# Kernel tuning notes

Measured on AMD Instinct MI355X. Metric: run time of the kernel, lower is better.

The kernel has to match this reference:

```python
import jax, jax.numpy as jnp
import numpy as np

D_MODEL = 2048
D_INNER = 4096
D_CONV = 4
D_STATE = 16
DT_RANK = 128  # (d_model + 15) // 16
EPS = 1e-5
B_SZ, SEQ = 2, 2048


def _silu(x):
    return x * jax.nn.sigmoid(x)


def setup_inputs() -> dict:
    key = jax.random.key(0)
    ks = jax.random.split(key, 10)
    s = lambda k, shape, sc=0.02: jax.random.normal(k, shape, jnp.float32) * sc
    # S4D-real init for A_log, small negative bias for dt (standard Mamba init)
    A_log = jnp.log(jnp.tile(jnp.arange(1, D_STATE + 1, dtype=jnp.float32), (D_INNER, 1)))
    return {
        "hidden_states": jax.random.normal(ks[0], (B_SZ, SEQ, D_MODEL), jnp.float32),
        "norm_scale": jnp.ones((D_MODEL,), jnp.float32),
        "in_proj_w": s(ks[1], (2 * D_INNER, D_MODEL)),
        "conv_w": s(ks[2], (D_INNER, 1, D_CONV), 0.1),
        "conv_b": s(ks[3], (D_INNER,), 0.1),
        "x_proj_w": s(ks[4], (DT_RANK + 2 * D_STATE, D_INNER)),
        "dt_proj_w": s(ks[5], (D_INNER, DT_RANK), 0.1),
        "dt_proj_b": jnp.full((D_INNER,), -4.0, jnp.float32) + s(ks[6], (D_INNER,), 0.1),
        "out_proj_w": s(ks[7], (D_MODEL, D_INNER)),
        "A_log": A_log,
        "D": jnp.ones((D_INNER,), jnp.float32),
    }


def reference(hidden_states, norm_scale, in_proj_w, conv_w, conv_b, x_proj_w,
              dt_proj_w, dt_proj_b, out_proj_w, A_log, D):
    B, L, _ = hidden_states.shape
    residual = hidden_states
    # RMSNorm
    rms = jnp.sqrt(jnp.mean(hidden_states ** 2, axis=-1, keepdims=True) + EPS)
    xn = hidden_states / rms * norm_scale
    # in_proj -> [B, L, 2*d_inner]; torch code keeps this as projected_states
    xz = jnp.einsum('bld,ed->ble', xn, in_proj_w)
    x_in = xz[..., :D_INNER].transpose(0, 2, 1)  # [B, d_inner, L]
    z = xz[..., D_INNER:]                        # [B, L, d_inner]
    # depthwise causal conv1d (padding d_conv-1, truncated to L) + SiLU
    xc = jax.lax.conv_general_dilated(
        x_in, conv_w, window_strides=(1,), padding=[(D_CONV - 1, 0)],
        feature_group_count=D_INNER)
    xc = _silu(xc + conv_b[None, :, None])       # [B, d_inner, L]
    # x_proj -> dt, B, C
    x_dbl = jnp.einsum('bdl,rd->brl', xc, x_proj_w)  # [B, dt_rank+2*d_state, L]
    dt_low = x_dbl[:, :DT_RANK]
    Bm = x_dbl[:, DT_RANK:DT_RANK + D_STATE]         # [B, d_state, L]
    Cm = x_dbl[:, DT_RANK + D_STATE:]                # [B, d_state, L]
    delta = jax.nn.softplus(
        jnp.einsum('dr,brl->bdl', dt_proj_w, dt_low) + dt_proj_b[None, :, None])
    A = -jnp.exp(A_log)                              # [d_inner, d_state]
    # selective scan: h_t = exp(delta_t * A) * h_{t-1} + delta_t * B_t * u_t
    delta_t = delta.transpose(2, 0, 1)  # [L, B, d_inner]
    u_t = xc.transpose(2, 0, 1)         # [L, B, d_inner]
    B_t = Bm.transpose(2, 0, 1)         # [L, B, d_state]
    C_t = Cm.transpose(2, 0, 1)         # [L, B, d_state]

    def step(h, inp):
        d_, b_, c_, u_ = inp
        dA = jnp.exp(d_[..., None] * A)                      # [B, d_inner, d_state]
        h = h * dA + (d_ * u_)[..., None] * b_[:, None, :]   # [B, d_inner, d_state]
        y = jnp.einsum('bds,bs->bd', h, c_)                  # [B, d_inner]
        return h, y

    h0 = jnp.zeros((B, D_INNER, D_STATE), hidden_states.dtype)
    _, ys = jax.lax.scan(step, h0, (delta_t, B_t, C_t, u_t))  # [L, B, d_inner]
    y = ys.transpose(1, 0, 2) + xc.transpose(0, 2, 1) * D     # [B, L, d_inner]
    y = y * _silu(z)
    out = jnp.einsum('bld,od->blo', y, out_proj_w)            # [B, L, d_model]
    return residual + out, xz
```

## Files before the change

### kernel.cpp

```cpp
#include <hip/hip_runtime.h>
#include <cstdint>
#include <cstddef>

#define DM   2048
#define DI   4096
#define DST  16
#define DTR  128
#define SEQL 2048
#define NTOK 4096
#define XZW  8192
#define NCHAIN 8192
#define CL   32
#define NCH  64

typedef short short8 __attribute__((ext_vector_type(8)));
typedef float f32x4 __attribute__((ext_vector_type(4)));

__device__ __forceinline__ short f2bf(float x) {
  union { float f; uint32_t u; } v; v.f = x;
  uint32_t r = v.u + 0x7fffu + ((v.u >> 16) & 1u);
  return (short)(r >> 16);
}
__device__ __forceinline__ float bf2f(short s) {
  union { uint32_t u; float f; } v; v.u = ((uint32_t)(uint16_t)s) << 16;
  return v.f;
}

__device__ __forceinline__ void stage16(const short* g, short* l) {
#if __has_builtin(__builtin_amdgcn_global_load_lds)
  __builtin_amdgcn_global_load_lds((const __attribute__((address_space(1))) void*)g,
                                   (__attribute__((address_space(3))) void*)l, 16, 0, 0);
#else
  *(short8*)l = *(const short8*)g;
#endif
}

#define NG_WIN  (XZW * DM / 4)
#define NG_WOUT (DM * DI / 4)
#define NG_WDT  (DI * DTR / 4)
#define NG_PAD  (256 * DI / 4)
#define NG_ALL  (NG_WIN + NG_WOUT + NG_WDT + NG_PAD)
#define NB_CVT  (NG_ALL / 256)
__global__ __launch_bounds__(256) void prep_k(const float* __restrict__ win,
                                              const float* __restrict__ wout,
                                              const float* __restrict__ wdt,
                                              const float* __restrict__ xp,
                                              const float* __restrict__ hs,
                                              const float* __restrict__ nsc,
                                              short* __restrict__ win_bf,
                                              short* __restrict__ wout_bf,
                                              short* __restrict__ wdt_bf,
                                              short* __restrict__ wxp_bf,
                                              short* __restrict__ xn_bf) {
  const int blk = blockIdx.x;
  const int tid = threadIdx.x;
  if (blk < NB_CVT) {
    const size_t i = (size_t)blk * 256 + tid;
    float4 v;
    short4* dst;
    if (i < NG_WIN) {
      v = ((const float4*)win)[i];
      dst = (short4*)win_bf + i;
    } else if (i < NG_WIN + NG_WOUT) {
      const size_t j = i - NG_WIN;
      v = ((const float4*)wout)[j];
      dst = (short4*)wout_bf + j;
    } else if (i < NG_WIN + NG_WOUT + NG_WDT) {
      const size_t j = i - NG_WIN - NG_WOUT;
      v = ((const float4*)wdt)[j];
      dst = (short4*)wdt_bf + j;
    } else {
      const size_t j = i - NG_WIN - NG_WOUT - NG_WDT;
      const int r = (int)(j >> 10);
      v = (r < 160) ? ((const float4*)xp)[j] : make_float4(0.f, 0.f, 0.f, 0.f);
      dst = (short4*)wxp_bf + j;
    }
    short4 o;
    o.x = f2bf(v.x); o.y = f2bf(v.y); o.z = f2bf(v.z); o.w = f2bf(v.w);
    *dst = o;
  } else {
    const int token = blk - NB_CVT;
    const float* row = hs + (size_t)token * DM;
    float4 a = ((const float4*)row)[tid];
    float4 b = ((const float4*)row)[tid + 256];
    float ss = a.x*a.x + a.y*a.y + a.z*a.z + a.w*a.w
             + b.x*b.x + b.y*b.y + b.z*b.z + b.w*b.w;
    #pragma unroll
    for (int o = 32; o > 0; o >>= 1) ss += __shfl_xor(ss, o);
    __shared__ float wsum[4];
    if ((tid & 63) == 0) wsum[tid >> 6] = ss;
    __syncthreads();
    float tot = wsum[0] + wsum[1] + wsum[2] + wsum[3];
    float inv = rsqrtf(tot * (1.0f / DM) + 1e-5f);
    float4 s1 = ((const float4*)nsc)[tid];
    float4 s2 = ((const float4*)nsc)[tid + 256];
    short4 o1, o2;
    o1.x = f2bf(a.x * inv * s1.x); o1.y = f2bf(a.y * inv * s1.y);
    o1.z = f2bf(a.z * inv * s1.z); o1.w = f2bf(a.w * inv * s1.w);
    o2.x = f2bf(b.x * inv * s2.x); o2.y = f2bf(b.y * inv * s2.y);
    o2.z = f2bf(b.z * inv * s2.z); o2.w = f2bf(b.w * inv * s2.w);
    ((short4*)xn_bf)[(size_t)token * (DM / 4) + tid] = o1;
    ((short4*)xn_bf)[(size_t)token * (DM / 4) + tid + 256] = o2;
  }
}

#define LGKM_FENCE() do { asm volatile("s_waitcnt lgkmcnt(0)" ::: "memory"); \
                          __builtin_amdgcn_sched_barrier(0); } while (0)

template <int RBY, int RBX>
__global__ __launch_bounds__(512) void gemm_big(const short* __restrict__ A,
                                                const short* __restrict__ B,
                                                int K, int ksz, int N, int nbx,
                                                float* __restrict__ out_f,
                                                size_t zstride) {
  constexpr int MFR = 8;
  constexpr int BM = 256;
  constexpr int ABYTES = BM * 128;
  constexpr int BBYTES = 256 * 128;
  constexpr int BUF = ABYTES + BBYTES;
  constexpr int FPP = 4;
  __shared__ char lds[2 * BUF];

  const int tid = threadIdx.x;
  const int lane = tid & 63;
  const int wid = tid >> 6;
  const int wm = wid >> 2;
  const int wn = wid & 3;
  const int lr = lane & 15;
  const int lj = lane >> 4;

  const int xcd = blockIdx.x & 7;
  const int idx = blockIdx.x >> 3;
  const int nrgx = nbx / RBX;
  const int by = (xcd / nrgx) * RBY + idx / RBX;
  const int bx = (xcd % nrgx) * RBX + idx % RBX;
  const size_t m0 = (size_t)by * BM;
  const size_t n0 = (size_t)bx * 256;

  const int kbase = blockIdx.y * ksz;
  out_f += (size_t)blockIdx.y * zstride;
  const int NT = ksz >> 6;

  auto stA1 = [&](int t, char* buf, int s) {
    const int k0 = kbase + (t << 6);
    const int off = s * 8192 + tid * 16;
    const int r = off >> 7;
    const int j = (off >> 4) & 7;
    stage16(A + (m0 + r) * (size_t)K + k0 + ((j ^ (r & 7)) << 3),
            (short*)(buf + off));
  };
  auto stB1 = [&](int t, char* buf, int s) {
    const int k0 = kbase + (t << 6);
    const int off = s * 8192 + tid * 16;
    const int r = off >> 7;
    const int j = (off >> 4) & 7;
    stage16(B + (n0 + r) * (size_t)K + k0 + ((j ^ (r & 7)) << 3),
            (short*)(buf + ABYTES + off));
  };

#define READ_A(dst, fbase)                                                   \
  _Pragma("unroll")                                                          \
  for (int f = 0; f < 4; ++f) {                                              \
    const int arow = wm * (BM / 2) + ((fbase) + f) * 16 + lr;                \
    _Pragma("unroll")                                                        \
    for (int ks = 0; ks < 2; ++ks)                                           \
      dst[f][ks] = *(const short8*)(cur + arow * 128 +                       \
                     ((((ks << 2) + lj) ^ (arow & 7)) << 4));                \
  }
#define READ_B(dst, gbase)                                                   \
  _Pragma("unroll")                                                          \
  for (int g = 0; g < 2; ++g) {                                              \
    const int brow = wn * 64 + ((gbase) + g) * 16 + lr;                      \
    _Pragma("unroll")                                                        \
    for (int ks = 0; ks < 2; ++ks)                                           \
      dst[g][ks] = *(const short8*)(cur + ABYTES + brow * 128 +              \
                     ((((ks << 2) + lj) ^ (brow & 7)) << 4));                \
  }
#define MFMA_Q(accoff, avoff, gbase, bvx)                                    \
  __builtin_amdgcn_s_setprio(1);                                             \
  _Pragma("unroll")                                                          \
  for (int ks = 0; ks < 2; ++ks)                                             \
    _Pragma("unroll")                                                        \
    for (int f = 0; f < FPP; ++f)                                            \
      _Pragma("unroll")                                                      \
      for (int g = 0; g < 2; ++g)                                            \
        acc[(accoff) + f][(gbase) + g] = __builtin_amdgcn_mfma_f32_16x16x32_bf16( \
            av[(avoff) + f][ks], bvx[g][ks], acc[(accoff) + f][(gbase) + g], 0, 0, 0); \
  __builtin_amdgcn_s_setprio(0);

  f32x4 acc[MFR][4] = {};

  {
    #pragma unroll
    for (int s = 0; s < 4; ++s) stA1(0, lds, s);
    #pragma unroll
    for (int s = 0; s < 4; ++s) stB1(0, lds, s);
    if (NT > 1) {
      stA1(1, lds + BUF, 0); stA1(1, lds + BUF, 2);
      asm volatile("s_waitcnt vmcnt(2)" ::: "memory");
    } else asm volatile("s_waitcnt vmcnt(0)" ::: "memory");
    __builtin_amdgcn_s_barrier();
    __builtin_amdgcn_sched_barrier(0);
  }

  for (int t = 0; t < NT; ++t) {
    char* cur = lds + (t & 1) * BUF;
    char* nxt = lds + ((t + 1) & 1) * BUF;
    const bool m1 = (t + 1) < NT;
    const bool m2 = (t + 2) < NT;
    short8 av[4][2], bv0[2][2], bv1[2][2];

    READ_A(av, 0);
    READ_B(bv0, 0);
    if (m1) { stA1(t + 1, nxt, 1); stA1(t + 1, nxt, 3); }
    LGKM_FENCE();
    MFMA_Q(0, 0, 0, bv0);
    __builtin_amdgcn_s_barrier();

    READ_B(bv1, 2);
    if (m1) { stB1(t + 1, nxt, 0); stB1(t + 1, nxt, 1); }
    LGKM_FENCE();
    MFMA_Q(0, 0, 2, bv1);
    __builtin_amdgcn_s_barrier();

    READ_A(av, 4);
    if (m1) { stB1(t + 1, nxt, 2); stB1(t + 1, nxt, 3); }
    if (m2) { stA1(t + 2, cur, 0); stA1(t + 2, cur, 2); }
    LGKM_FENCE();
    MFMA_Q(4, 0, 2, bv1);
    __builtin_amdgcn_s_barrier();

    MFMA_Q(4, 0, 0, bv0);
    if (m2) asm volatile("s_waitcnt vmcnt(2)" ::: "memory");
    else    asm volatile("s_waitcnt vmcnt(0)" ::: "memory");
    __builtin_amdgcn_s_barrier();
    __builtin_amdgcn_sched_barrier(0);
  }

  #pragma unroll
  for (int f = 0; f < MFR; ++f)
    #pragma unroll
    for (int g = 0; g < 4; ++g)
      #pragma unroll
      for (int jj = 0; jj < 4; ++jj) {
        const size_t row = m0 + wm * (BM / 2) + f * 16 + lj * 4 + jj;
        const size_t col = n0 + wn * 64 + g * 16 + lr;
        out_f[row * (size_t)N + col] = acc[f][g][jj];
      }
#undef READ_A
#undef READ_B
#undef MFMA_Q
}

__global__ __launch_bounds__(256) void combine_k(const float* __restrict__ part,
                                                 const float* __restrict__ hs,
                                                 float* __restrict__ out0) {
  const size_t i = (size_t)blockIdx.x * 256 + threadIdx.x;
  const float4 p0 = ((const float4*)part)[i];
  const float4 p1 = ((const float4*)part)[i + (size_t)NTOK * DM / 4];
  const float4 r  = ((const float4*)hs)[i];
  float4 o;
  o.x = r.x + p0.x + p1.x; o.y = r.y + p0.y + p1.y;
  o.z = r.z + p0.z + p1.z; o.w = r.w + p0.w + p1.w;
  ((float4*)out0)[i] = o;
}

template <int EPI>
__global__ __launch_bounds__(256) void gemm_nt(const short* __restrict__ A,
                                               const short* __restrict__ B,
                                               int ld, int K, int N,
                                               float* __restrict__ out_f,
                                               const float* __restrict__ aux_f,
                                               short* __restrict__ out_bf) {
  __shared__ short As[128 * 64];
  __shared__ short Bs[128 * 64];
  const int tid = threadIdx.x;
  const int lane = tid & 63;
  const int wid = tid >> 6;
  const int wr = wid >> 1, wc = wid & 1;
  const size_t m0 = (size_t)blockIdx.y * 128;
  const size_t n0 = (size_t)blockIdx.x * 128;
  A += (size_t)blockIdx.z * K;
  B += (size_t)blockIdx.z * K;
  f32x4 acc[4][4] = {};
  for (int k0 = 0; k0 < K; k0 += 64) {
    #pragma unroll
    for (int i = 0; i < 4; ++i) {
      const int off = i * 4096 + tid * 16;
      const int r = off >> 7;
      const int ke = (off & 127) >> 1;
      stage16(A + (m0 + r) * (size_t)ld + k0 + ke, &As[off >> 1]);
      stage16(B + (n0 + r) * (size_t)ld + k0 + ke, &Bs[off >> 1]);
    }
    __syncthreads();
    #pragma unroll
    for (int kk = 0; kk < 64; kk += 32) {
      short8 af[4], bfr[4];
      const int kb = kk + (lane >> 4) * 8;
      const int rr = lane & 15;
      #pragma unroll
      for (int f = 0; f < 4; ++f) {
        af[f]  = *(const short8*)&As[(wr * 64 + f * 16 + rr) * 64 + kb];
        bfr[f] = *(const short8*)&Bs[(wc * 64 + f * 16 + rr) * 64 + kb];
      }
      #pragma unroll
      for (int fm = 0; fm < 4; ++fm)
        #pragma unroll
        for (int fn = 0; fn < 4; ++fn)
          acc[fm][fn] = __builtin_amdgcn_mfma_f32_16x16x32_bf16(af[fm], bfr[fn], acc[fm][fn], 0, 0, 0);
    }
    __syncthreads();
  }
  const int rbase = (lane >> 4) * 4;
  const int cbase = lane & 15;
  #pragma unroll
  for (int fm = 0; fm < 4; ++fm) {
    #pragma unroll
    for (int fn = 0; fn < 4; ++fn) {
      #pragma unroll
      for (int j = 0; j < 4; ++j) {
        const size_t row = m0 + wr * 64 + fm * 16 + rbase + j;
        const size_t col = n0 + wc * 64 + fn * 16 + cbase;
        const float v = acc[fm][fn][j];
        if constexpr (EPI == 2) {
          float x = v + aux_f[col];
          float sp = (x > 20.f) ? x : log1pf(__expf(x));
          out_bf[row * (size_t)N + col] = f2bf(sp);
        } else {
          if (col < 160)
            out_f[((size_t)blockIdx.z * NTOK + row) * (size_t)N + col] = v;
        }
      }
    }
  }
}

__global__ __launch_bounds__(256) void xdbl_epi_k(const float* __restrict__ part,
                                                  short* __restrict__ dtl,
                                                  float* __restrict__ Bc,
                                                  float* __restrict__ Cc) {
  const int row = blockIdx.x;
  const int col = threadIdx.x;
  if (col >= 160) return;
  const size_t i = (size_t)row * 256 + col;
  const float v = part[i] + part[(size_t)NTOK * 256 + i]
                + part[(size_t)2 * NTOK * 256 + i]
                + part[(size_t)3 * NTOK * 256 + i];
  if (col < 128)      dtl[(size_t)row * 128 + col] = f2bf(v);
  else if (col < 144) Bc[(size_t)row * 16 + (col - 128)] = v;
  else                Cc[(size_t)row * 16 + (col - 144)] = v;
}

__global__ __launch_bounds__(256) void conv_silu_k(const float* __restrict__ xz,
                                                   const float* __restrict__ cw,
                                                   const float* __restrict__ cb,
                                                   short* __restrict__ xc) {
  const int d = blockIdx.x * 256 + threadIdx.x;
  const int t0 = blockIdx.y * 8;
  const int l0 = t0 & (SEQL - 1);
  const float4 w = ((const float4*)cw)[d];
  const float bias = cb[d];
  float x0 = (l0 >= 3) ? xz[(size_t)(t0 - 3) * XZW + d] : 0.f;
  float x1 = (l0 >= 2) ? xz[(size_t)(t0 - 2) * XZW + d] : 0.f;
  float x2 = (l0 >= 1) ? xz[(size_t)(t0 - 1) * XZW + d] : 0.f;
  #pragma unroll
  for (int i = 0; i < 8; ++i) {
    const float x3 = xz[(size_t)(t0 + i) * XZW + d];
    const float acc = bias + w.x * x0 + w.y * x1 + w.z * x2 + w.w * x3;
    const float sv = acc / (1.f + __expf(-acc));
    xc[(size_t)(t0 + i) * DI + d] = f2bf(sv);
    x0 = x1; x1 = x2; x2 = x3;
  }
}

__global__ __launch_bounds__(256) void scan1_k(const short* __restrict__ del_bf,
                                               const short* __restrict__ xc,
                                               const float* __restrict__ Bc,
                                               const float* __restrict__ alog,
                                               float* __restrict__ hloc,
                                               float* __restrict__ Ssum) {
  const int t = blockIdx.x * 256 + threadIdx.x;
  const int sub = t & 1;
  const int chain = (t >> 1) & (NCHAIN - 1);
  const int chunk = t >> 14;
  const int b = chain >> 12;
  const int d = chain & 4095;
  float A[8];
  #pragma unroll
  for (int j = 0; j < 8; ++j) A[j] = -__expf(alog[d * 16 + sub * 8 + j]);
  float h[8] = {};
  float S = 0.f;
  size_t token = (size_t)b * SEQL + (size_t)chunk * CL;
  #pragma unroll 2
  for (int l = 0; l < CL; ++l, ++token) {
    const float delta = bf2f(del_bf[token * DI + d]);
    const float u = bf2f(xc[token * DI + d]);
    const float du = delta * u;
    S += delta;
    const float4 B0 = ((const float4*)Bc)[token * 4 + sub * 2];
    const float4 B1 = ((const float4*)Bc)[token * 4 + sub * 2 + 1];
    const float Bv[8] = {B0.x, B0.y, B0.z, B0.w, B1.x, B1.y, B1.z, B1.w};
    #pragma unroll
    for (int j = 0; j < 8; ++j)
      h[j] = h[j] * __expf(delta * A[j]) + du * Bv[j];
  }
  const size_t idx = (size_t)(chunk * NCHAIN + chain) * 4 + sub * 2;
  ((float4*)hloc)[idx]     = make_float4(h[0], h[1], h[2], h[3]);
  ((float4*)hloc)[idx + 1] = make_float4(h[4], h[5], h[6], h[7]);
  if (sub == 0) Ssum[chunk * NCHAIN + chain] = S;
}

__global__ __launch_bounds__(256) void scan2_k(float* __restrict__ hloc,
                                               const float* __restrict__ Ssum,
                                               const float* __restrict__ alog) {
  const int t = blockIdx.x * 256 + threadIdx.x;
  const int q = t & 3;
  const int chain = t >> 2;
  const int d = chain & 4095;
  float A[4];
  #pragma unroll
  for (int j = 0; j < 4; ++j) A[j] = -__expf(alog[d * 16 + q * 4 + j]);
  float4 h = make_float4(0.f, 0.f, 0.f, 0.f);
  for (int c = 0; c < NCH; ++c) {
    const size_t idx = (size_t)(c * NCHAIN + chain) * 4 + q;
    const float S = Ssum[c * NCHAIN + chain];
    const float4 hl = ((const float4*)hloc)[idx];
    ((float4*)hloc)[idx] = h;
    h.x = h.x * __expf(A[0] * S) + hl.x;
    h.y = h.y * __expf(A[1] * S) + hl.y;
    h.z = h.z * __expf(A[2] * S) + hl.z;
    h.w = h.w * __expf(A[3] * S) + hl.w;
  }
}

__global__ __launch_bounds__(256) void scan3_k(const short* __restrict__ del_bf,
                                               const short* __restrict__ xc,
                                               const float* __restrict__ Bc,
                                               const float* __restrict__ Cc,
                                               const float* __restrict__ xzbuf,
                                               const float* __restrict__ alog,
                                               const float* __restrict__ dvec,
                                               const float* __restrict__ hin,
                                               short* __restrict__ y) {
  const int t = blockIdx.x * 256 + threadIdx.x;
  const int sub = t & 1;
  const int chain = (t >> 1) & (NCHAIN - 1);
  const int chunk = t >> 14;
  const int b = chain >> 12;
  const int d = chain & 4095;
  float A[8];
  #pragma unroll
  for (int j = 0; j < 8; ++j) A[j] = -__expf(alog[d * 16 + sub * 8 + j]);
  const float Dd = dvec[d];
  const size_t idx = (size_t)(chunk * NCHAIN + chain) * 4 + sub * 2;
  const float4 h0 = ((const float4*)hin)[idx];
  const float4 h1 = ((const float4*)hin)[idx + 1];
  float h[8] = {h0.x, h0.y, h0.z, h0.w, h1.x, h1.y, h1.z, h1.w};
  size_t token = (size_t)b * SEQL + (size_t)chunk * CL;
  #pragma unroll 2
  for (int l = 0; l < CL; ++l, ++token) {
    const float delta = bf2f(del_bf[token * DI + d]);
    const float u = bf2f(xc[token * DI + d]);
    const float du = delta * u;
    const float4 B0 = ((const float4*)Bc)[token * 4 + sub * 2];
    const float4 B1 = ((const float4*)Bc)[token * 4 + sub * 2 + 1];
    const float4 C0 = ((const float4*)Cc)[token * 4 + sub * 2];
    const float4 C1 = ((const float4*)Cc)[token * 4 + sub * 2 + 1];
    const float Bv[8] = {B0.x, B0.y, B0.z, B0.w, B1.x, B1.y, B1.z, B1.w};
    const float Cv[8] = {C0.x, C0.y, C0.z, C0.w, C1.x, C1.y, C1.z, C1.w};
    float yp = 0.f;
    #pragma unroll
    for (int j = 0; j < 8; ++j) {
      h[j] = h[j] * __expf(delta * A[j]) + du * Bv[j];
      yp += h[j] * Cv[j];
    }
    yp += __shfl_xor(yp, 1);
    if (sub == 0) {
      const float z = xzbuf[token * XZW + DI + d];
      const float sz = z / (1.f + __expf(-z));
      y[token * DI + d] = f2bf((yp + u * Dd) * sz);
    }
  }
}

extern "C" void kernel_launch(void* const* d_in, const int* in_sizes, int n_in,
                              void* d_out, int out_size, void* d_ws, size_t ws_size,
                              hipStream_t stream) {
  const float* hs   = (const float*)d_in[0];
  const float* nsc  = (const float*)d_in[1];
  const float* win  = (const float*)d_in[2];
  const float* cw   = (const float*)d_in[3];
  const float* cb   = (const float*)d_in[4];
  const float* wxp  = (const float*)d_in[5];
  const float* wdt  = (const float*)d_in[6];
  const float* bdt  = (const float*)d_in[7];
  const float* wout = (const float*)d_in[8];
  const float* alog = (const float*)d_in[9];
  const float* dvec = (const float*)d_in[10];

  float* out0 = (float*)d_out;
  float* xz   = out0 + (size_t)NTOK * DM;

  char* w = (char*)d_ws;
  size_t off = 0;
  auto alloc = [&](size_t bytes) {
    char* p = w + off;
    off += (bytes + 255) & ~(size_t)255;
    return p;
  };
  short* xn_bf   = (short*)alloc((size_t)NTOK * DM * 2);
  short* win_bf  = (short*)alloc((size_t)XZW * DM * 2);
  short* wout_bf = (short*)alloc((size_t)DM * DI * 2);
  short* wdt_bf  = (short*)alloc((size_t)DI * DTR * 2);
  short* wxp_bf  = (short*)alloc((size_t)256 * DI * 2);
  short* xc_bf   = (short*)alloc((size_t)NTOK * DI * 2);
  short* dtl_bf  = (short*)alloc((size_t)NTOK * DTR * 2);
  float* Bc      = (float*)alloc((size_t)NTOK * DST * 4);
  float* Cc      = (float*)alloc((size_t)NTOK * DST * 4);
  short* del_bf  = (short*)alloc((size_t)NTOK * DI * 2);
  short* y_bf    = (short*)alloc((size_t)NTOK * DI * 2);

  float* xp_part = (float*)win_bf;
  float* hloc    = (float*)win_bf;
  float* Ssum    = (float*)xn_bf;
  float* opart   = (float*)xc_bf;

  prep_k<<<NB_CVT + NTOK, 256, 0, stream>>>(
      win, wout, wdt, wxp, hs, nsc, win_bf, wout_bf, wdt_bf, wxp_bf, xn_bf);
  gemm_big<8, 8><<<dim3((XZW / 256) * (NTOK / 256)), 512, 0, stream>>>(
      xn_bf, win_bf, DM, DM, XZW, XZW / 256, xz, 0);
  conv_silu_k<<<dim3(DI / 256, NTOK / 8), 256, 0, stream>>>(xz, cw, cb, xc_bf);
  gemm_nt<4><<<dim3(2, NTOK / 128, 4), 256, 0, stream>>>(
      xc_bf, wxp_bf, DI, DI / 4, 256, xp_part, nullptr, nullptr);
  xdbl_epi_k<<<NTOK, 256, 0, stream>>>(xp_part, dtl_bf, Bc, Cc);
  gemm_nt<2><<<dim3(DI / 128, NTOK / 128, 1), 256, 0, stream>>>(
      dtl_bf, wdt_bf, DTR, DTR, DI, nullptr, bdt, del_bf);
  scan1_k<<<(NCHAIN * 2 * NCH) / 256, 256, 0, stream>>>(
      del_bf, xc_bf, Bc, alog, hloc, Ssum);
  scan2_k<<<(NCHAIN * 4) / 256, 256, 0, stream>>>(hloc, Ssum, alog);
  scan3_k<<<(NCHAIN * 2 * NCH) / 256, 256, 0, stream>>>(
      del_bf, xc_bf, Bc, Cc, xz, alog, dvec, hloc, y_bf);
  gemm_big<4, 4><<<dim3((DM / 256) * (NTOK / 256), 2), 512, 0, stream>>>(
      y_bf, wout_bf, DI, DI / 2, DM, DM / 256, opart, (size_t)NTOK * DM);
  combine_k<<<(NTOK * DM / 4) / 256, 256, 0, stream>>>(opart, hs, out0);
}
```

Measured before the change: 554.9 us.

## Give each scan thread all 16 states and run dt_proj through the big GEMM

The scan1/scan3 kernels now assign one thread per chain with all 16 SSM states instead of splitting the states across two threads. This removes the cross-lane shuffle and the duplicated delta/u/z loads, and halves the thread count. The dt_proj GEMM (K=128) moves from the 128x128 gemm_nt kernel to the 256-wide gemm_big template, which gains a softplus epilogue. The risks are higher register pressure and lower occupancy in the scan, and the big GEMM's pipeline being poorly suited to such a short K.

```diff
diff --git a/kernel.cpp b/kernel.cpp
--- a/kernel.cpp
+++ b/kernel.cpp
@@ -107,12 +107,14 @@
 #define LGKM_FENCE() do { asm volatile("s_waitcnt lgkmcnt(0)" ::: "memory"); \
                           __builtin_amdgcn_sched_barrier(0); } while (0)
 
-template <int RBY, int RBX>
+template <int RBY, int RBX, int EPI>
 __global__ __launch_bounds__(512) void gemm_big(const short* __restrict__ A,
                                                 const short* __restrict__ B,
                                                 int K, int ksz, int N, int nbx,
                                                 float* __restrict__ out_f,
-                                                size_t zstride) {
+                                                size_t zstride,
+                                                const float* __restrict__ aux,
+                                                short* __restrict__ out_bf) {
   constexpr int MFR = 8;
   constexpr int BM = 256;
   constexpr int ABYTES = BM * 128;
@@ -245,7 +247,13 @@
       for (int jj = 0; jj < 4; ++jj) {
         const size_t row = m0 + wm * (BM / 2) + f * 16 + lj * 4 + jj;
         const size_t col = n0 + wn * 64 + g * 16 + lr;
-        out_f[row * (size_t)N + col] = acc[f][g][jj];
+        if constexpr (EPI == 0) {
+          out_f[row * (size_t)N + col] = acc[f][g][jj];
+        } else {
+          float x = acc[f][g][jj] + aux[col];
+          float sp = (x > 20.f) ? x : log1pf(__expf(x));
+          out_bf[row * (size_t)N + col] = f2bf(sp);
+        }
       }
 #undef READ_A
 #undef READ_B
@@ -265,13 +273,10 @@
   ((float4*)out0)[i] = o;
 }
 
-template <int EPI>
-__global__ __launch_bounds__(256) void gemm_nt(const short* __restrict__ A,
-                                               const short* __restrict__ B,
-                                               int ld, int K, int N,
-                                               float* __restrict__ out_f,
-                                               const float* __restrict__ aux_f,
-                                               short* __restrict__ out_bf) {
+__global__ __launch_bounds__(256) void gemm_nt4(const short* __restrict__ A,
+                                                const short* __restrict__ B,
+                                                int ld, int K, int N,
+                                                float* __restrict__ out_f) {
   __shared__ short As[128 * 64];
   __shared__ short Bs[128 * 64];
   const int tid = threadIdx.x;
@@ -321,15 +326,8 @@
       for (int j = 0; j < 4; ++j) {
         const size_t row = m0 + wr * 64 + fm * 16 + rbase + j;
         const size_t col = n0 + wc * 64 + fn * 16 + cbase;
-        const float v = acc[fm][fn][j];
-        if constexpr (EPI == 2) {
-          float x = v + aux_f[col];
-          float sp = (x > 20.f) ? x : log1pf(__expf(x));
-          out_bf[row * (size_t)N + col] = f2bf(sp);
-        } else {
-          if (col < 160)
-            out_f[((size_t)blockIdx.z * NTOK + row) * (size_t)N + col] = v;
-        }
+        if (col < 160)
+          out_f[((size_t)blockIdx.z * NTOK + row) * (size_t)N + col] = acc[fm][fn][j];
       }
     }
   }
@@ -373,6 +371,8 @@
   }
 }
 
+#define H_STEP(hj, Aj, Bv)  hj = hj * __expf(delta * Aj) + du * Bv
+
 __global__ __launch_bounds__(256) void scan1_k(const short* __restrict__ del_bf,
                                                const short* __restrict__ xc,
                                                const float* __restrict__ Bc,
@@ -380,15 +380,14 @@
                                                float* __restrict__ hloc,
                                                float* __restrict__ Ssum) {
   const int t = blockIdx.x * 256 + threadIdx.x;
-  const int sub = t & 1;
-  const int chain = (t >> 1) & (NCHAIN - 1);
-  const int chunk = t >> 14;
+  const int chain = t & (NCHAIN - 1);
+  const int chunk = t >> 13;
   const int b = chain >> 12;
   const int d = chain & 4095;
-  float A[8];
+  float A[16];
   #pragma unroll
-  for (int j = 0; j < 8; ++j) A[j] = -__expf(alog[d * 16 + sub * 8 + j]);
-  float h[8] = {};
+  for (int j = 0; j < 16; ++j) A[j] = -__expf(alog[d * 16 + j]);
+  float h[16] = {};
   float S = 0.f;
   size_t token = (size_t)b * SEQL + (size_t)chunk * CL;
   #pragma unroll 2
@@ -397,17 +396,25 @@
     const float u = bf2f(xc[token * DI + d]);
     const float du = delta * u;
     S += delta;
-    const float4 B0 = ((const float4*)Bc)[token * 4 + sub * 2];
-    const float4 B1 = ((const float4*)Bc)[token * 4 + sub * 2 + 1];
-    const float Bv[8] = {B0.x, B0.y, B0.z, B0.w, B1.x, B1.y, B1.z, B1.w};
-    #pragma unroll
-    for (int j = 0; j < 8; ++j)
-      h[j] = h[j] * __expf(delta * A[j]) + du * Bv[j];
-  }
-  const size_t idx = (size_t)(chunk * NCHAIN + chain) * 4 + sub * 2;
-  ((float4*)hloc)[idx]     = make_float4(h[0], h[1], h[2], h[3]);
+    const float4 B0 = ((const float4*)Bc)[token * 4 + 0];
+    H_STEP(h[0], A[0], B0.x); H_STEP(h[1], A[1], B0.y);
+    H_STEP(h[2], A[2], B0.z); H_STEP(h[3], A[3], B0.w);
+    const float4 B1 = ((const float4*)Bc)[token * 4 + 1];
+    H_STEP(h[4], A[4], B1.x); H_STEP(h[5], A[5], B1.y);
+    H_STEP(h[6], A[6], B1.z); H_STEP(h[7], A[7], B1.w);
+    const float4 B2 = ((const float4*)Bc)[token * 4 + 2];
+    H_STEP(h[8], A[8], B2.x); H_STEP(h[9], A[9], B2.y);
+    H_STEP(h[10], A[10], B2.z); H_STEP(h[11], A[11], B2.w);
+    const float4 B3 = ((const float4*)Bc)[token * 4 + 3];
+    H_STEP(h[12], A[12], B3.x); H_STEP(h[13], A[13], B3.y);
+    H_STEP(h[14], A[14], B3.z); H_STEP(h[15], A[15], B3.w);
+  }
+  const size_t idx = (size_t)(chunk * NCHAIN + chain) * 4;
+  ((float4*)hloc)[idx + 0] = make_float4(h[0], h[1], h[2], h[3]);
   ((float4*)hloc)[idx + 1] = make_float4(h[4], h[5], h[6], h[7]);
-  if (sub == 0) Ssum[chunk * NCHAIN + chain] = S;
+  ((float4*)hloc)[idx + 2] = make_float4(h[8], h[9], h[10], h[11]);
+  ((float4*)hloc)[idx + 3] = make_float4(h[12], h[13], h[14], h[15]);
+  Ssum[chunk * NCHAIN + chain] = S;
 }
 
 __global__ __launch_bounds__(256) void scan2_k(float* __restrict__ hloc,
@@ -443,43 +450,68 @@
                                                const float* __restrict__ hin,
                                                short* __restrict__ y) {
   const int t = blockIdx.x * 256 + threadIdx.x;
-  const int sub = t & 1;
-  const int chain = (t >> 1) & (NCHAIN - 1);
-  const int chunk = t >> 14;
+  const int chain = t & (NCHAIN - 1);
+  const int chunk = t >> 13;
   const int b = chain >> 12;
   const int d = chain & 4095;
-  float A[8];
+  float A[16];
   #pragma unroll
-  for (int j = 0; j < 8; ++j) A[j] = -__expf(alog[d * 16 + sub * 8 + j]);
+  for (int j = 0; j < 16; ++j) A[j] = -__expf(alog[d * 16 + j]);
   const float Dd = dvec[d];
-  const size_t idx = (size_t)(chunk * NCHAIN + chain) * 4 + sub * 2;
-  const float4 h0 = ((const float4*)hin)[idx];
-  const float4 h1 = ((const float4*)hin)[idx + 1];
-  float h[8] = {h0.x, h0.y, h0.z, h0.w, h1.x, h1.y, h1.z, h1.w};
+  const size_t idx = (size_t)(chunk * NCHAIN + chain) * 4;
+  float h[16];
+  {
+    const float4 h0 = ((const float4*)hin)[idx + 0];
+    const float4 h1 = ((const float4*)hin)[idx + 1];
+    const float4 h2 = ((const float4*)hin)[idx + 2];
+    const float4 h3 = ((const float4*)hin)[idx + 3];
+    h[0]=h0.x; h[1]=h0.y; h[2]=h0.z; h[3]=h0.w;
+    h[4]=h1.x; h[5]=h1.y; h[6]=h1.z; h[7]=h1.w;
+    h[8]=h2.x; h[9]=h2.y; h[10]=h2.z; h[11]=h2.w;
+    h[12]=h3.x; h[13]=h3.y; h[14]=h3.z; h[15]=h3.w;
+  }
   size_t token = (size_t)b * SEQL + (size_t)chunk * CL;
   #pragma unroll 2
   for (int l = 0; l < CL; ++l, ++token) {
     const float delta = bf2f(del_bf[token * DI + d]);
     const float u = bf2f(xc[token * DI + d]);
     const float du = delta * u;
-    const float4 B0 = ((const float4*)Bc)[token * 4 + sub * 2];
-    const float4 B1 = ((const float4*)Bc)[token * 4 + sub * 2 + 1];
-    const float4 C0 = ((const float4*)Cc)[token * 4 + sub * 2];
-    const float4 C1 = ((const float4*)Cc)[token * 4 + sub * 2 + 1];
-    const float Bv[8] = {B0.x, B0.y, B0.z, B0.w, B1.x, B1.y, B1.z, B1.w};
-    const float Cv[8] = {C0.x, C0.y, C0.z, C0.w, C1.x, C1.y, C1.z, C1.w};
     float yp = 0.f;
-    #pragma unroll
-    for (int j = 0; j < 8; ++j) {
-      h[j] = h[j] * __expf(delta * A[j]) + du * Bv[j];
-      yp += h[j] * Cv[j];
-    }
-    yp += __shfl_xor(yp, 1);
-    if (sub == 0) {
-      const float z = xzbuf[token * XZW + DI + d];
-      const float sz = z / (1.f + __expf(-z));
-      y[token * DI + d] = f2bf((yp + u * Dd) * sz);
-    }
+    {
+      const float4 B0 = ((const float4*)Bc)[token * 4 + 0];
+      const float4 C0 = ((const float4*)Cc)[token * 4 + 0];
+      H_STEP(h[0], A[0], B0.x); yp += h[0] * C0.x;
+      H_STEP(h[1], A[1], B0.y); yp += h[1] * C0.y;
+      H_STEP(h[2], A[2], B0.z); yp += h[2] * C0.z;
+      H_STEP(h[3], A[3], B0.w); yp += h[3] * C0.w;
+    }
+    {
+      const float4 B1 = ((const float4*)Bc)[token * 4 + 1];
+      const float4 C1 = ((const float4*)Cc)[token * 4 + 1];
+      H_STEP(h[4], A[4], B1.x); yp += h[4] * C1.x;
+      H_STEP(h[5], A[5], B1.y); yp += h[5] * C1.y;
+      H_STEP(h[6], A[6], B1.z); yp += h[6] * C1.z;
+      H_STEP(h[7], A[7], B1.w); yp += h[7] * C1.w;
+    }
+    {
+      const float4 B2 = ((const float4*)Bc)[token * 4 + 2];
+      const float4 C2 = ((const float4*)Cc)[token * 4 + 2];
+      H_STEP(h[8], A[8], B2.x);  yp += h[8] * C2.x;
+      H_STEP(h[9], A[9], B2.y);  yp += h[9] * C2.y;
+      H_STEP(h[10], A[10], B2.z); yp += h[10] * C2.z;
+      H_STEP(h[11], A[11], B2.w); yp += h[11] * C2.w;
+    }
+    {
+      const float4 B3 = ((const float4*)Bc)[token * 4 + 3];
+      const float4 C3 = ((const float4*)Cc)[token * 4 + 3];
+      H_STEP(h[12], A[12], B3.x); yp += h[12] * C3.x;
+      H_STEP(h[13], A[13], B3.y); yp += h[13] * C3.y;
+      H_STEP(h[14], A[14], B3.z); yp += h[14] * C3.z;
+      H_STEP(h[15], A[15], B3.w); yp += h[15] * C3.w;
+    }
+    const float z = xzbuf[token * XZW + DI + d];
+    const float sz = z / (1.f + __expf(-z));
+    y[token * DI + d] = f2bf((yp + u * Dd) * sz);
   }
 }
 
@@ -527,20 +559,21 @@
 
   prep_k<<<NB_CVT + NTOK, 256, 0, stream>>>(
       win, wout, wdt, wxp, hs, nsc, win_bf, wout_bf, wdt_bf, wxp_bf, xn_bf);
-  gemm_big<8, 8><<<dim3((XZW / 256) * (NTOK / 256)), 512, 0, stream>>>(
-      xn_bf, win_bf, DM, DM, XZW, XZW / 256, xz, 0);
+  gemm_big<8, 8, 0><<<dim3((XZW / 256) * (NTOK / 256)), 512, 0, stream>>>(
+      xn_bf, win_bf, DM, DM, XZW, XZW / 256, xz, 0, nullptr, nullptr);
   conv_silu_k<<<dim3(DI / 256, NTOK / 8), 256, 0, stream>>>(xz, cw, cb, xc_bf);
-  gemm_nt<4><<<dim3(2, NTOK / 128, 4), 256, 0, stream>>>(
-      xc_bf, wxp_bf, DI, DI / 4, 256, xp_part, nullptr, nullptr);
+  gemm_nt4<<<dim3(2, NTOK / 128, 4), 256, 0, stream>>>(
+      xc_bf, wxp_bf, DI, DI / 4, 256, xp_part);
   xdbl_epi_k<<<NTOK, 256, 0, stream>>>(xp_part, dtl_bf, Bc, Cc);
-  gemm_nt<2><<<dim3(DI / 128, NTOK / 128, 1), 256, 0, stream>>>(
-      dtl_bf, wdt_bf, DTR, DTR, DI, nullptr, bdt, del_bf);
-  scan1_k<<<(NCHAIN * 2 * NCH) / 256, 256, 0, stream>>>(
+  gemm_big<8, 4, 1><<<dim3((DI / 256) * (NTOK / 256)), 512, 0, stream>>>(
+      dtl_bf, wdt_bf, DTR, DTR, DI, DI / 256, nullptr, 0, bdt, del_bf);
+  scan1_k<<<(NCHAIN * NCH) / 256, 256, 0, stream>>>(
       del_bf, xc_bf, Bc, alog, hloc, Ssum);
   scan2_k<<<(NCHAIN * 4) / 256, 256, 0, stream>>>(hloc, Ssum, alog);
-  scan3_k<<<(NCHAIN * 2 * NCH) / 256, 256, 0, stream>>>(
+  scan3_k<<<(NCHAIN * NCH) / 256, 256, 0, stream>>>(
       del_bf, xc_bf, Bc, Cc, xz, alog, dvec, hloc, y_bf);
-  gemm_big<4, 4><<<dim3((DM / 256) * (NTOK / 256), 2), 512, 0, stream>>>(
-      y_bf, wout_bf, DI, DI / 2, DM, DM / 256, opart, (size_t)NTOK * DM);
+  gemm_big<4, 4, 0><<<dim3((DM / 256) * (NTOK / 256), 2), 512, 0, stream>>>(
+      y_bf, wout_bf, DI, DI / 2, DM, DM / 256, opart, (size_t)NTOK * DM,
+      nullptr, nullptr);
   combine_k<<<(NTOK * DM / 4) / 256, 256, 0, stream>>>(opart, hs, out0);
 }
```

Measured after the change: 625.0 us. 12.6% more time.
